# Kernel optimization log

Hardware: AMD Instinct MI355X
Metric: run time of the kernel (lower is better)

Reference implementation:

```python
import jax, jax.numpy as jnp
import numpy as np

D_MODEL = 768
NUM_HEADS = 12
D_K = D_MODEL // NUM_HEADS


def setup_inputs() -> dict:
    key = jax.random.key(0)
    ks = jax.random.split(key, 9)
    B, S = 2, 4096
    s = 1.0 / np.sqrt(D_MODEL).astype(np.float32)
    inp = {
        "x": jax.random.normal(ks[0], (B, S, D_MODEL), dtype=jnp.float32),
        "wq": jax.random.normal(ks[1], (D_MODEL, D_MODEL), dtype=jnp.float32) * s,
        "bq": jnp.zeros((D_MODEL,), dtype=jnp.float32),
        "wk": jax.random.normal(ks[2], (D_MODEL, D_MODEL), dtype=jnp.float32) * s,
        "bk": jnp.zeros((D_MODEL,), dtype=jnp.float32),
        "wv": jax.random.normal(ks[3], (D_MODEL, D_MODEL), dtype=jnp.float32) * s,
        "bv": jnp.zeros((D_MODEL,), dtype=jnp.float32),
        "wo": jax.random.normal(ks[4], (D_MODEL, D_MODEL), dtype=jnp.float32) * s,
        "bo": jnp.zeros((D_MODEL,), dtype=jnp.float32),
    }
    return inp


def reference(x, wq, bq, wk, bk, wv, bv, wo, bo):
    B, S, D = x.shape
    H, dk = NUM_HEADS, D_K
    # projections (torch Linear: x @ W^T + b); weights here stored as [in, out]
    def proj(w, b):
        y = jnp.einsum("bsd,df->bsf", x, w) + b
        return y.reshape(B, S, H, dk).transpose(0, 2, 1, 3)  # [B,H,S,dk]
    q = proj(wq, bq)
    k = proj(wk, bk)
    v = proj(wv, bv)
    scores = jnp.einsum("bhqd,bhkd->bhqk", q, k) / np.sqrt(dk).astype(np.float32)
    attn = jax.nn.softmax(scores, axis=-1)  # dropout is identity in eval
    out = jnp.einsum("bhqk,bhkd->bhqd", attn, v)
    out = out.transpose(0, 2, 1, 3).reshape(B, S, D)
    return jnp.einsum("bsd,df->bsf", out, wo) + bo
```

## Files before the change

kernel.cpp:

```cpp
#include <hip/hip_runtime.h>

typedef unsigned short u16;
typedef unsigned int u32;
typedef __bf16 bf16x8 __attribute__((ext_vector_type(8)));
typedef short s16x4 __attribute__((ext_vector_type(4)));
typedef float f32x4 __attribute__((ext_vector_type(4)));

#define AS1(p) ((const __attribute__((address_space(1))) void*)(p))
#define AS3(p) ((__attribute__((address_space(3))) void*)(p))

__device__ __forceinline__ u16 f2bf(float f) {
    u32 u = __float_as_uint(f);
    u += 0x7fffu + ((u >> 16) & 1u);
    return (u16)(u >> 16);
}

__device__ __forceinline__ short bfbits(float f) {
    __bf16 h = (__bf16)f;
    return __builtin_bit_cast(short, h);
}

#define NXQ 6291456

__global__ __launch_bounds__(256) void prep_kernel(
    const float* __restrict__ x,
    const float* __restrict__ wq, const float* __restrict__ wk,
    const float* __restrict__ wv, const float* __restrict__ wo,
    const float* __restrict__ bq, const float* __restrict__ bk,
    const float* __restrict__ bv,
    u16* __restrict__ xbf, u16* __restrict__ WT, float* __restrict__ bqkv)
{
    const int t = threadIdx.x;
    const int bid = blockIdx.x;
    if (bid < 6144) {
        int i = bid * 256 + t;
        float4 v = ((const float4*)x)[i];
        uint2 o;
        o.x = (u32)f2bf(v.x) | ((u32)f2bf(v.y) << 16);
        o.y = (u32)f2bf(v.z) | ((u32)f2bf(v.w) << 16);
        ((uint2*)xbf)[i] = o;
        return;
    }
    int tb = bid - 6144;
    int mat = tb / 144;
    int tt = tb - mat * 144;
    int tr = tt / 12, tc = tt - tr * 12;
    const float* W = (mat == 0) ? wq : (mat == 1) ? wk : (mat == 2) ? wv : wo;
    __shared__ u16 sT[64 * 72];
    #pragma unroll
    for (int rr = 0; rr < 4; ++rr) {
        int r = (t >> 4) + rr * 16;
        int cb = (t & 15) * 4;
        float4 v = *(const float4*)&W[(size_t)(tr * 64 + r) * 768 + tc * 64 + cb];
        sT[(cb + 0) * 72 + r] = f2bf(v.x);
        sT[(cb + 1) * 72 + r] = f2bf(v.y);
        sT[(cb + 2) * 72 + r] = f2bf(v.z);
        sT[(cb + 3) * 72 + r] = f2bf(v.w);
    }
    __syncthreads();
    #pragma unroll
    for (int i = 0; i < 2; ++i) {
        int nr = t >> 2;
        int cc = (t & 3) * 16 + i * 8;
        *(uint4*)&WT[(size_t)(mat * 768 + tc * 64 + nr) * 768 + tr * 64 + cc] =
            *(uint4*)&sT[nr * 72 + cc];
    }
    if (tb < 9) {
        int i = tb * 256 + t;
        if (i < 2304)
            bqkv[i] = (i < 768) ? bq[i] : (i < 1536) ? bk[i - 768] : bv[i - 1536];
    }
}

template<int MODE>
__global__ __launch_bounds__(256, 4) void gemm_kernel(
    const u16* __restrict__ A, const u16* __restrict__ WT,
    const float* __restrict__ bias, void* __restrict__ out)
{
    __shared__ u16 sA[128 * 64];
    __shared__ u16 sB[128 * 64];

    const int m0 = blockIdx.x * 128;
    const int n0g = blockIdx.y * 128;
    const int tid = threadIdx.x, lane = tid & 63, wave = tid >> 6;
    const int quad = lane >> 4, l16 = lane & 15;
    const int wm = (wave & 1) * 64, wn = (wave >> 1) * 64;

    f32x4 acc[4][4];
    #pragma unroll
    for (int i = 0; i < 4; ++i)
        #pragma unroll
        for (int j = 0; j < 4; ++j)
            #pragma unroll
            for (int r = 0; r < 4; ++r)
                acc[i][j][r] = 0.f;

    const int srow = (lane >> 3);
    const int skc = ((lane & 7) ^ (srow & 7)) * 8;

    for (int k0 = 0; k0 < 768; k0 += 64) {
        __syncthreads();
        #pragma unroll
        for (int i = 0; i < 4; ++i) {
            int c = wave * 4 + i;
            int row = c * 8 + srow;
            __builtin_amdgcn_global_load_lds(
                AS1(&A[(size_t)(m0 + row) * 768 + k0 + (((lane & 7) ^ (row & 7)) * 8)]),
                AS3(&sA[c * 512]), 16, 0, 0);
            __builtin_amdgcn_global_load_lds(
                AS1(&WT[(size_t)(n0g + row) * 768 + k0 + (((lane & 7) ^ (row & 7)) * 8)]),
                AS3(&sB[c * 512]), 16, 0, 0);
        }
        __syncthreads();
        #pragma unroll
        for (int s = 0; s < 2; ++s) {
            bf16x8 af[4], bfr[4];
            #pragma unroll
            for (int i = 0; i < 4; ++i) {
                int row = wm + i * 16 + l16;
                af[i] = *(const bf16x8*)&sA[row * 64 + (((s * 4 + quad) ^ (row & 7)) * 8)];
            }
            #pragma unroll
            for (int j = 0; j < 4; ++j) {
                int row = wn + j * 16 + l16;
                bfr[j] = *(const bf16x8*)&sB[row * 64 + (((s * 4 + quad) ^ (row & 7)) * 8)];
            }
            #pragma unroll
            for (int i = 0; i < 4; ++i)
                #pragma unroll
                for (int j = 0; j < 4; ++j)
                    acc[i][j] = __builtin_amdgcn_mfma_f32_16x16x32_bf16(af[i], bfr[j], acc[i][j], 0, 0, 0);
        }
    }

    if (MODE == 0) {
        const int mat = blockIdx.y / 6;
        const int nm0 = n0g - mat * 768;
        const float scale = (mat == 0) ? 0.125f : 1.0f;
        u16* dst = (u16*)out + (size_t)mat * NXQ;
        #pragma unroll
        for (int i = 0; i < 4; ++i) {
            #pragma unroll
            for (int j = 0; j < 4; ++j) {
                int colg = n0g + wn + j * 16 + l16;
                int col = nm0 + wn + j * 16 + l16;
                float bv = bias[colg];
                int h = col >> 6, d = col & 63;
                int row0 = m0 + wm + i * 16 + quad * 4;
                int b = row0 >> 12, s = row0 & 4095;
                if (mat < 2) {
                    #pragma unroll
                    for (int r = 0; r < 4; ++r)
                        dst[(((size_t)(b * 12 + h) * 4096) + s + r) * 64 + d] =
                            f2bf((acc[i][j][r] + bv) * scale);
                } else {
                    ushort4 w;
                    w.x = f2bf(acc[i][j][0] + bv);
                    w.y = f2bf(acc[i][j][1] + bv);
                    w.z = f2bf(acc[i][j][2] + bv);
                    w.w = f2bf(acc[i][j][3] + bv);
                    *(ushort4*)&dst[(((size_t)(b * 12 + h) * 64 + d) * 4096) + s] = w;
                }
            }
        }
    } else {
        #pragma unroll
        for (int i = 0; i < 4; ++i) {
            #pragma unroll
            for (int j = 0; j < 4; ++j) {
                int col = n0g + wn + j * 16 + l16;
                float bv = bias[col];
                #pragma unroll
                for (int r = 0; r < 4; ++r) {
                    int row = m0 + wm + i * 16 + quad * 4 + r;
                    ((float*)out)[(size_t)row * 768 + col] = acc[i][j][r] + bv;
                }
            }
        }
    }
}

__global__ __launch_bounds__(256, 2) void flash_kernel(
    const u16* __restrict__ Q, const u16* __restrict__ K,
    const u16* __restrict__ Vt, u16* __restrict__ O)
{
    const int bh = blockIdx.y;
    const int q0 = blockIdx.x * 128;
    const u16* Qp = Q + (size_t)bh * 4096 * 64;
    const u16* Kp = K + (size_t)bh * 4096 * 64;
    const u16* Vp = Vt + (size_t)bh * 64 * 4096;
    const int tid = threadIdx.x, lane = tid & 63, wave = tid >> 6;
    const int quad = lane >> 4, l16 = lane & 15;

    __shared__ u16 sK[2][64 * 64];
    __shared__ u16 sVT[2][64 * 64];

    const int qrow = q0 + wave * 32;
    bf16x8 qf[2][2];
    #pragma unroll
    for (int i = 0; i < 2; ++i)
        #pragma unroll
        for (int s = 0; s < 2; ++s)
            qf[i][s] = *(const bf16x8*)&Qp[(size_t)(qrow + i * 16 + l16) * 64 + s * 32 + quad * 8];

    f32x4 oacc[4][2];
    float lrun[2] = {0.f, 0.f};
    #pragma unroll
    for (int jd = 0; jd < 4; ++jd)
        #pragma unroll
        for (int i = 0; i < 2; ++i)
            #pragma unroll
            for (int r = 0; r < 4; ++r)
                oacc[jd][i][r] = 0.f;

    const int srow = lane >> 3;
    auto stage = [&](int t, int buf) {
        #pragma unroll
        for (int i = 0; i < 2; ++i) {
            int c = wave * 2 + i;
            int row = c * 8 + srow;
            int kc = ((lane & 7) ^ (row & 7)) * 8;
            __builtin_amdgcn_global_load_lds(
                AS1(&Kp[(size_t)(t * 64 + row) * 64 + kc]),
                AS3(&sK[buf][c * 512]), 16, 0, 0);
            __builtin_amdgcn_global_load_lds(
                AS1(&Vp[(size_t)row * 4096 + t * 64 + kc]),
                AS3(&sVT[buf][c * 512]), 16, 0, 0);
        }
    };

    stage(0, 0);

    for (int t = 0; t < 64; ++t) {
        __syncthreads();
        if (t + 1 < 64) stage(t + 1, (t + 1) & 1);
        const int cur = t & 1;

        f32x4 sacc[4][2];
        #pragma unroll
        for (int m = 0; m < 4; ++m)
            #pragma unroll
            for (int i = 0; i < 2; ++i)
                #pragma unroll
                for (int r = 0; r < 4; ++r)
                    sacc[m][i][r] = 0.f;
        #pragma unroll
        for (int s = 0; s < 2; ++s) {
            bf16x8 ak[4];
            #pragma unroll
            for (int m = 0; m < 4; ++m) {
                int row = m * 16 + l16;
                ak[m] = *(const bf16x8*)&sK[cur][row * 64 + (((s * 4 + quad) ^ (row & 7)) * 8)];
            }
            #pragma unroll
            for (int m = 0; m < 4; ++m)
                #pragma unroll
                for (int i = 0; i < 2; ++i)
                    sacc[m][i] = __builtin_amdgcn_mfma_f32_16x16x32_bf16(ak[m], qf[i][s], sacc[m][i], 0, 0, 0);
        }

        s16x4 bp[4][2];
        #pragma unroll
        for (int i = 0; i < 2; ++i) {
            #pragma unroll
            for (int kk = 0; kk < 4; ++kk) {
                float p0 = __expf(sacc[kk][i][0]);
                float p1 = __expf(sacc[kk][i][1]);
                float p2 = __expf(sacc[kk][i][2]);
                float p3 = __expf(sacc[kk][i][3]);
                lrun[i] += (p0 + p1) + (p2 + p3);
                s16x4 b;
                b[0] = bfbits(p0); b[1] = bfbits(p1);
                b[2] = bfbits(p2); b[3] = bfbits(p3);
                bp[kk][i] = b;
            }
        }

        #pragma unroll
        for (int kk = 0; kk < 4; ++kk) {
            s16x4 av[4];
            #pragma unroll
            for (int jd = 0; jd < 4; ++jd) {
                int row = jd * 16 + l16;
                av[jd] = *(const s16x4*)&sVT[cur][row * 64 +
                            (((kk * 2 + (quad >> 1)) ^ (row & 7)) * 8) + (quad & 1) * 4];
            }
            #pragma unroll
            for (int jd = 0; jd < 4; ++jd)
                #pragma unroll
                for (int i = 0; i < 2; ++i)
                    oacc[jd][i] = __builtin_amdgcn_mfma_f32_16x16x16bf16_1k(av[jd], bp[kk][i], oacc[jd][i], 0, 0, 0);
        }
    }

    #pragma unroll
    for (int i = 0; i < 2; ++i) {
        lrun[i] += __shfl_xor(lrun[i], 16);
        lrun[i] += __shfl_xor(lrun[i], 32);
    }

    const int b = bh / 12, h = bh - b * 12;
    #pragma unroll
    for (int i = 0; i < 2; ++i) {
        float inv = 1.0f / lrun[i];
        int s = qrow + i * 16 + l16;
        #pragma unroll
        for (int jd = 0; jd < 4; ++jd) {
            ushort4 w;
            w.x = f2bf(oacc[jd][i][0] * inv);
            w.y = f2bf(oacc[jd][i][1] * inv);
            w.z = f2bf(oacc[jd][i][2] * inv);
            w.w = f2bf(oacc[jd][i][3] * inv);
            *(ushort4*)&O[((size_t)(b * 4096 + s)) * 768 + h * 64 + jd * 16 + quad * 4] = w;
        }
    }
}

extern "C" void kernel_launch(void* const* d_in, const int* in_sizes, int n_in,
                              void* d_out, int out_size, void* d_ws, size_t ws_size,
                              hipStream_t stream)
{
    (void)in_sizes; (void)n_in; (void)out_size; (void)ws_size;
    const float* x  = (const float*)d_in[0];
    const float* wq = (const float*)d_in[1];
    const float* bq = (const float*)d_in[2];
    const float* wk = (const float*)d_in[3];
    const float* bk = (const float*)d_in[4];
    const float* wv = (const float*)d_in[5];
    const float* bv = (const float*)d_in[6];
    const float* wo = (const float*)d_in[7];
    const float* bo = (const float*)d_in[8];
    float* out = (float*)d_out;

    u16* ws = (u16*)d_ws;
    u16* xbf = ws;
    u16* WT  = xbf + (size_t)8192 * 768;
    u16* Qb  = WT + (size_t)3072 * 768;
    u16* Kb  = Qb + NXQ;
    u16* Vtb = Kb + NXQ;
    u16* Ob  = Vtb + NXQ;
    float* bqkv = (float*)(Ob + NXQ);

    prep_kernel<<<6720, 256, 0, stream>>>(x, wq, wk, wv, wo, bq, bk, bv, xbf, WT, bqkv);
    gemm_kernel<0><<<dim3(64, 18), 256, 0, stream>>>(xbf, WT, bqkv, Qb);
    flash_kernel<<<dim3(32, 24), 256, 0, stream>>>(Qb, Kb, Vtb, Ob);
    gemm_kernel<1><<<dim3(64, 6), 256, 0, stream>>>(Ob, WT + (size_t)2304 * 768, bo, out);
}
```

Measured before the change: 300.5 us.

## Double-buffer GEMMs, split out-projection kernel, use exp2 and MFMA row sums in flash

The QKV GEMM is rewritten to use a BK=32 double-buffered LDS pipeline, and the output projection becomes its own kernel with 64-row tiles, doubling its grid. In the flash kernel, Q is pre-scaled by log2(e)/8 so exp2 can replace expf. The softmax denominator is now computed by an MFMA against a ones vector instead of scalar adds and shuffles, and the attention loop is unrolled by two for static buffer indices. These changes aim to hide global load latency and cut VALU work, at the cost of an extra MFMA per step, more syncs per K step, and smaller GEMM tiles.

```diff
diff --git a/kernel.cpp b/kernel.cpp
--- a/kernel.cpp
+++ b/kernel.cpp
@@ -9,6 +9,12 @@
 #define AS1(p) ((const __attribute__((address_space(1))) void*)(p))
 #define AS3(p) ((__attribute__((address_space(3))) void*)(p))
 
+#if __has_builtin(__builtin_amdgcn_exp2f)
+#define EXP2(x) __builtin_amdgcn_exp2f(x)
+#else
+#define EXP2(x) __builtin_exp2f(x)
+#endif
+
 __device__ __forceinline__ u16 f2bf(float f) {
     u32 u = __float_as_uint(f);
     u += 0x7fffu + ((u >> 16) & 1u);
@@ -21,6 +27,7 @@
 }
 
 #define NXQ 6291456
+#define QSCALE 0.1803368801111249f
 
 __global__ __launch_bounds__(256) void prep_kernel(
     const float* __restrict__ x,
@@ -72,14 +79,12 @@
     }
 }
 
-template<int MODE>
-__global__ __launch_bounds__(256, 4) void gemm_kernel(
+__global__ __launch_bounds__(256, 4) void gemm_qkv(
     const u16* __restrict__ A, const u16* __restrict__ WT,
-    const float* __restrict__ bias, void* __restrict__ out)
+    const float* __restrict__ bias, u16* __restrict__ out)
 {
-    __shared__ u16 sA[128 * 64];
-    __shared__ u16 sB[128 * 64];
-
+    __shared__ u16 sA[2][128 * 32];
+    __shared__ u16 sB[2][128 * 32];
     const int m0 = blockIdx.x * 128;
     const int n0g = blockIdx.y * 128;
     const int tid = threadIdx.x, lane = tid & 63, wave = tid >> 6;
@@ -95,86 +100,166 @@
             for (int r = 0; r < 4; ++r)
                 acc[i][j][r] = 0.f;
 
-    const int srow = (lane >> 3);
-    const int skc = ((lane & 7) ^ (srow & 7)) * 8;
-
-    for (int k0 = 0; k0 < 768; k0 += 64) {
-        __syncthreads();
+    const int srow = lane >> 2;
+    const int scc = lane & 3;
+
+    auto stage = [&](int k0, int buf) {
+        #pragma unroll
+        for (int i = 0; i < 2; ++i) {
+            int c = wave * 2 + i;
+            int row = c * 16 + srow;
+            int kc = (scc ^ (row & 3)) * 8;
+            __builtin_amdgcn_global_load_lds(
+                AS1(&A[(size_t)(m0 + row) * 768 + k0 + kc]),
+                AS3(&sA[buf][c * 512]), 16, 0, 0);
+            __builtin_amdgcn_global_load_lds(
+                AS1(&WT[(size_t)(n0g + row) * 768 + k0 + kc]),
+                AS3(&sB[buf][c * 512]), 16, 0, 0);
+        }
+    };
+
+    auto compute = [&](int buf) {
+        bf16x8 af[4], bfr[4];
         #pragma unroll
         for (int i = 0; i < 4; ++i) {
-            int c = wave * 4 + i;
-            int row = c * 8 + srow;
-            __builtin_amdgcn_global_load_lds(
-                AS1(&A[(size_t)(m0 + row) * 768 + k0 + (((lane & 7) ^ (row & 7)) * 8)]),
-                AS3(&sA[c * 512]), 16, 0, 0);
-            __builtin_amdgcn_global_load_lds(
-                AS1(&WT[(size_t)(n0g + row) * 768 + k0 + (((lane & 7) ^ (row & 7)) * 8)]),
-                AS3(&sB[c * 512]), 16, 0, 0);
-        }
-        __syncthreads();
-        #pragma unroll
-        for (int s = 0; s < 2; ++s) {
-            bf16x8 af[4], bfr[4];
-            #pragma unroll
-            for (int i = 0; i < 4; ++i) {
-                int row = wm + i * 16 + l16;
-                af[i] = *(const bf16x8*)&sA[row * 64 + (((s * 4 + quad) ^ (row & 7)) * 8)];
-            }
-            #pragma unroll
-            for (int j = 0; j < 4; ++j) {
-                int row = wn + j * 16 + l16;
-                bfr[j] = *(const bf16x8*)&sB[row * 64 + (((s * 4 + quad) ^ (row & 7)) * 8)];
-            }
-            #pragma unroll
-            for (int i = 0; i < 4; ++i)
+            int row = wm + i * 16 + l16;
+            af[i] = *(const bf16x8*)&sA[buf][row * 32 + ((quad ^ (row & 3)) * 8)];
+        }
+        #pragma unroll
+        for (int j = 0; j < 4; ++j) {
+            int row = wn + j * 16 + l16;
+            bfr[j] = *(const bf16x8*)&sB[buf][row * 32 + ((quad ^ (row & 3)) * 8)];
+        }
+        #pragma unroll
+        for (int i = 0; i < 4; ++i)
+            #pragma unroll
+            for (int j = 0; j < 4; ++j)
+                acc[i][j] = __builtin_amdgcn_mfma_f32_16x16x32_bf16(af[i], bfr[j], acc[i][j], 0, 0, 0);
+    };
+
+    stage(0, 0);
+    for (int kt = 0; kt < 24; kt += 2) {
+        __syncthreads();
+        stage((kt + 1) * 32, 1);
+        compute(0);
+        __syncthreads();
+        if (kt + 2 < 24) stage((kt + 2) * 32, 0);
+        compute(1);
+    }
+
+    const int mat = blockIdx.y / 6;
+    const int nm0 = n0g - mat * 768;
+    const float scale = (mat == 0) ? QSCALE : 1.0f;
+    u16* dst = out + (size_t)mat * NXQ;
+    #pragma unroll
+    for (int i = 0; i < 4; ++i) {
+        #pragma unroll
+        for (int j = 0; j < 4; ++j) {
+            int colg = n0g + wn + j * 16 + l16;
+            int col = nm0 + wn + j * 16 + l16;
+            float bv = bias[colg];
+            int h = col >> 6, d = col & 63;
+            int row0 = m0 + wm + i * 16 + quad * 4;
+            int b = row0 >> 12, s = row0 & 4095;
+            if (mat < 2) {
                 #pragma unroll
-                for (int j = 0; j < 4; ++j)
-                    acc[i][j] = __builtin_amdgcn_mfma_f32_16x16x32_bf16(af[i], bfr[j], acc[i][j], 0, 0, 0);
-        }
-    }
-
-    if (MODE == 0) {
-        const int mat = blockIdx.y / 6;
-        const int nm0 = n0g - mat * 768;
-        const float scale = (mat == 0) ? 0.125f : 1.0f;
-        u16* dst = (u16*)out + (size_t)mat * NXQ;
-        #pragma unroll
-        for (int i = 0; i < 4; ++i) {
-            #pragma unroll
-            for (int j = 0; j < 4; ++j) {
-                int colg = n0g + wn + j * 16 + l16;
-                int col = nm0 + wn + j * 16 + l16;
-                float bv = bias[colg];
-                int h = col >> 6, d = col & 63;
-                int row0 = m0 + wm + i * 16 + quad * 4;
-                int b = row0 >> 12, s = row0 & 4095;
-                if (mat < 2) {
-                    #pragma unroll
-                    for (int r = 0; r < 4; ++r)
-                        dst[(((size_t)(b * 12 + h) * 4096) + s + r) * 64 + d] =
-                            f2bf((acc[i][j][r] + bv) * scale);
-                } else {
-                    ushort4 w;
-                    w.x = f2bf(acc[i][j][0] + bv);
-                    w.y = f2bf(acc[i][j][1] + bv);
-                    w.z = f2bf(acc[i][j][2] + bv);
-                    w.w = f2bf(acc[i][j][3] + bv);
-                    *(ushort4*)&dst[(((size_t)(b * 12 + h) * 64 + d) * 4096) + s] = w;
-                }
-            }
-        }
-    } else {
-        #pragma unroll
-        for (int i = 0; i < 4; ++i) {
-            #pragma unroll
-            for (int j = 0; j < 4; ++j) {
-                int col = n0g + wn + j * 16 + l16;
-                float bv = bias[col];
-                #pragma unroll
-                for (int r = 0; r < 4; ++r) {
-                    int row = m0 + wm + i * 16 + quad * 4 + r;
-                    ((float*)out)[(size_t)row * 768 + col] = acc[i][j][r] + bv;
-                }
+                for (int r = 0; r < 4; ++r)
+                    dst[(((size_t)(b * 12 + h) * 4096) + s + r) * 64 + d] =
+                        f2bf((acc[i][j][r] + bv) * scale);
+            } else {
+                ushort4 w;
+                w.x = f2bf(acc[i][j][0] + bv);
+                w.y = f2bf(acc[i][j][1] + bv);
+                w.z = f2bf(acc[i][j][2] + bv);
+                w.w = f2bf(acc[i][j][3] + bv);
+                *(ushort4*)&dst[(((size_t)(b * 12 + h) * 64 + d) * 4096) + s] = w;
+            }
+        }
+    }
+}
+
+__global__ __launch_bounds__(256, 4) void gemm_out(
+    const u16* __restrict__ A, const u16* __restrict__ WT,
+    const float* __restrict__ bias, float* __restrict__ out)
+{
+    __shared__ u16 sA[2][64 * 32];
+    __shared__ u16 sB[2][128 * 32];
+    const int m0 = blockIdx.x * 64;
+    const int n0 = blockIdx.y * 128;
+    const int tid = threadIdx.x, lane = tid & 63, wave = tid >> 6;
+    const int quad = lane >> 4, l16 = lane & 15;
+    const int wm = (wave & 1) * 32, wn = (wave >> 1) * 64;
+
+    f32x4 acc[2][4];
+    #pragma unroll
+    for (int i = 0; i < 2; ++i)
+        #pragma unroll
+        for (int j = 0; j < 4; ++j)
+            #pragma unroll
+            for (int r = 0; r < 4; ++r)
+                acc[i][j][r] = 0.f;
+
+    const int srow = lane >> 2;
+    const int scc = lane & 3;
+
+    auto stage = [&](int k0, int buf) {
+        {
+            int row = wave * 16 + srow;
+            int kc = (scc ^ (row & 3)) * 8;
+            __builtin_amdgcn_global_load_lds(
+                AS1(&A[(size_t)(m0 + row) * 768 + k0 + kc]),
+                AS3(&sA[buf][wave * 512]), 16, 0, 0);
+        }
+        #pragma unroll
+        for (int i = 0; i < 2; ++i) {
+            int c = wave * 2 + i;
+            int row = c * 16 + srow;
+            int kc = (scc ^ (row & 3)) * 8;
+            __builtin_amdgcn_global_load_lds(
+                AS1(&WT[(size_t)(n0 + row) * 768 + k0 + kc]),
+                AS3(&sB[buf][c * 512]), 16, 0, 0);
+        }
+    };
+
+    auto compute = [&](int buf) {
+        bf16x8 af[2], bfr[4];
+        #pragma unroll
+        for (int i = 0; i < 2; ++i) {
+            int row = wm + i * 16 + l16;
+            af[i] = *(const bf16x8*)&sA[buf][row * 32 + ((quad ^ (row & 3)) * 8)];
+        }
+        #pragma unroll
+        for (int j = 0; j < 4; ++j) {
+            int row = wn + j * 16 + l16;
+            bfr[j] = *(const bf16x8*)&sB[buf][row * 32 + ((quad ^ (row & 3)) * 8)];
+        }
+        #pragma unroll
+        for (int i = 0; i < 2; ++i)
+            #pragma unroll
+            for (int j = 0; j < 4; ++j)
+                acc[i][j] = __builtin_amdgcn_mfma_f32_16x16x32_bf16(af[i], bfr[j], acc[i][j], 0, 0, 0);
+    };
+
+    stage(0, 0);
+    for (int kt = 0; kt < 24; kt += 2) {
+        __syncthreads();
+        stage((kt + 1) * 32, 1);
+        compute(0);
+        __syncthreads();
+        if (kt + 2 < 24) stage((kt + 2) * 32, 0);
+        compute(1);
+    }
+
+    #pragma unroll
+    for (int i = 0; i < 2; ++i) {
+        #pragma unroll
+        for (int j = 0; j < 4; ++j) {
+            int col = n0 + wn + j * 16 + l16;
+            float bv = bias[col];
+            #pragma unroll
+            for (int r = 0; r < 4; ++r) {
+                int row = m0 + wm + i * 16 + quad * 4 + r;
+                out[(size_t)row * 768 + col] = acc[i][j][r] + bv;
             }
         }
     }
@@ -204,7 +289,7 @@
             qf[i][s] = *(const bf16x8*)&Qp[(size_t)(qrow + i * 16 + l16) * 64 + s * 32 + quad * 8];
 
     f32x4 oacc[4][2];
-    float lrun[2] = {0.f, 0.f};
+    f32x4 lacc[2];
     #pragma unroll
     for (int jd = 0; jd < 4; ++jd)
         #pragma unroll
@@ -212,6 +297,15 @@
             #pragma unroll
             for (int r = 0; r < 4; ++r)
                 oacc[jd][i][r] = 0.f;
+    #pragma unroll
+    for (int i = 0; i < 2; ++i)
+        #pragma unroll
+        for (int r = 0; r < 4; ++r)
+            lacc[i][r] = 0.f;
+
+    s16x4 ones;
+    #pragma unroll
+    for (int r = 0; r < 4; ++r) ones[r] = (short)0x3F80;
 
     const int srow = lane >> 3;
     auto stage = [&](int t, int buf) {
@@ -229,13 +323,7 @@
         }
     };
 
-    stage(0, 0);
-
-    for (int t = 0; t < 64; ++t) {
-        __syncthreads();
-        if (t + 1 < 64) stage(t + 1, (t + 1) & 1);
-        const int cur = t & 1;
-
+    auto body = [&](int cur) {
         f32x4 sacc[4][2];
         #pragma unroll
         for (int m = 0; m < 4; ++m)
@@ -264,14 +352,11 @@
         for (int i = 0; i < 2; ++i) {
             #pragma unroll
             for (int kk = 0; kk < 4; ++kk) {
-                float p0 = __expf(sacc[kk][i][0]);
-                float p1 = __expf(sacc[kk][i][1]);
-                float p2 = __expf(sacc[kk][i][2]);
-                float p3 = __expf(sacc[kk][i][3]);
-                lrun[i] += (p0 + p1) + (p2 + p3);
                 s16x4 b;
-                b[0] = bfbits(p0); b[1] = bfbits(p1);
-                b[2] = bfbits(p2); b[3] = bfbits(p3);
+                b[0] = bfbits(EXP2(sacc[kk][i][0]));
+                b[1] = bfbits(EXP2(sacc[kk][i][1]));
+                b[2] = bfbits(EXP2(sacc[kk][i][2]));
+                b[3] = bfbits(EXP2(sacc[kk][i][3]));
                 bp[kk][i] = b;
             }
         }
@@ -286,23 +371,29 @@
                             (((kk * 2 + (quad >> 1)) ^ (row & 7)) * 8) + (quad & 1) * 4];
             }
             #pragma unroll
-            for (int jd = 0; jd < 4; ++jd)
+            for (int i = 0; i < 2; ++i) {
                 #pragma unroll
-                for (int i = 0; i < 2; ++i)
+                for (int jd = 0; jd < 4; ++jd)
                     oacc[jd][i] = __builtin_amdgcn_mfma_f32_16x16x16bf16_1k(av[jd], bp[kk][i], oacc[jd][i], 0, 0, 0);
-        }
-    }
-
+                lacc[i] = __builtin_amdgcn_mfma_f32_16x16x16bf16_1k(ones, bp[kk][i], lacc[i], 0, 0, 0);
+            }
+        }
+    };
+
+    stage(0, 0);
+    for (int t = 0; t < 64; t += 2) {
+        __syncthreads();
+        stage(t + 1, 1);
+        body(0);
+        __syncthreads();
+        if (t + 2 < 64) stage(t + 2, 0);
+        body(1);
+    }
+
+    const int b = bh / 12, h = bh - b * 12;
     #pragma unroll
     for (int i = 0; i < 2; ++i) {
-        lrun[i] += __shfl_xor(lrun[i], 16);
-        lrun[i] += __shfl_xor(lrun[i], 32);
-    }
-
-    const int b = bh / 12, h = bh - b * 12;
-    #pragma unroll
-    for (int i = 0; i < 2; ++i) {
-        float inv = 1.0f / lrun[i];
+        float inv = 1.0f / lacc[i][0];
         int s = qrow + i * 16 + l16;
         #pragma unroll
         for (int jd = 0; jd < 4; ++jd) {
@@ -342,7 +433,7 @@
     float* bqkv = (float*)(Ob + NXQ);
 
     prep_kernel<<<6720, 256, 0, stream>>>(x, wq, wk, wv, wo, bq, bk, bv, xbf, WT, bqkv);
-    gemm_kernel<0><<<dim3(64, 18), 256, 0, stream>>>(xbf, WT, bqkv, Qb);
+    gemm_qkv<<<dim3(64, 18), 256, 0, stream>>>(xbf, WT, bqkv, Qb);
     flash_kernel<<<dim3(32, 24), 256, 0, stream>>>(Qb, Kb, Vtb, Ob);
-    gemm_kernel<1><<<dim3(64, 6), 256, 0, stream>>>(Ob, WT + (size_t)2304 * 768, bo, out);
-}
+    gemm_out<<<dim3(128, 6), 256, 0, stream>>>(Ob, WT + (size_t)2304 * 768, bo, out);
+}
```

New measurement: 286.4 us. 4.7% less time.
